# Kernel tuning notes

Hardware: AMD Instinct MI355X
Metric: run time of the kernel (lower is better)

The kernel has to match this reference:

```python
import jax, jax.numpy as jnp
import numpy as np

H, E, K, T_ENC = 512, 256, 256, 256  # hidden, embed, output_size(tags), max_length

def setup_inputs() -> dict:
    key = jax.random.key(0)
    ks = jax.random.split(key, 16)
    B, T = 128, 256
    s = 0.02
    return {
        "decoder_input": jax.random.randint(ks[0], (1, B, 1), 0, K),
        "output_tensor": jax.random.randint(ks[1], (T, B), 0, K),
        "encoder_outputs": jax.random.normal(ks[2], (T_ENC, B, 2 * H), dtype=jnp.float32),
        "emb": jax.random.normal(ks[3], (K, E), dtype=jnp.float32) * s,
        "attn_W": jax.random.normal(ks[4], (T_ENC, H + E), dtype=jnp.float32) * s,
        "attn_b": jnp.zeros((T_ENC,), jnp.float32),
        "comb_W": jax.random.normal(ks[5], (H, 2 * H + E), dtype=jnp.float32) * s,
        "comb_b": jnp.zeros((H,), jnp.float32),
        "gru_Wih": jax.random.normal(ks[6], (3 * H, H), dtype=jnp.float32) * s,
        "gru_Whh": jax.random.normal(ks[7], (3 * H, H), dtype=jnp.float32) * s,
        "gru_bih": jnp.zeros((3 * H,), jnp.float32),
        "gru_bhh": jnp.zeros((3 * H,), jnp.float32),
        "out_W": jax.random.normal(ks[8], (K, H), dtype=jnp.float32) * s,
        "out_b": jnp.zeros((K,), jnp.float32),
        "crf_start": jax.random.normal(ks[9], (K,), dtype=jnp.float32) * 0.1,
        "crf_end": jax.random.normal(ks[10], (K,), dtype=jnp.float32) * 0.1,
        "crf_trans": jax.random.normal(ks[11], (K, K), dtype=jnp.float32) * 0.1,
    }

def reference(decoder_input, output_tensor, encoder_outputs, emb, attn_W, attn_b,
              comb_W, comb_b, gru_Wih, gru_Whh, gru_bih, gru_bhh, out_W, out_b,
              crf_start, crf_end, crf_trans):
    B = decoder_input.shape[1]
    enc = jnp.transpose(encoder_outputs, (1, 0, 2))  # (B, T_enc, 2H)

    def dec_step(carry, true_t):
        dec_in, h = carry  # (B,), (B,H)
        e = emb[dec_in]  # (B,E)  (dropout_p=0 -> identity)
        aw = jax.nn.softmax(jnp.concatenate([e, h], axis=1) @ attn_W.T + attn_b, axis=1)  # (B,T_enc)
        ctx = jnp.einsum('bt,bth->bh', aw, enc)  # (B,2H)
        x = jax.nn.relu(jnp.concatenate([e, ctx], axis=1) @ comb_W.T + comb_b)  # (B,H)
        gi = x @ gru_Wih.T + gru_bih
        gh = h @ gru_Whh.T + gru_bhh
        ir, iz, inn = jnp.split(gi, 3, axis=1)
        hr, hz, hn = jnp.split(gh, 3, axis=1)
        r = jax.nn.sigmoid(ir + hr)
        z = jax.nn.sigmoid(iz + hz)
        n = jnp.tanh(inn + r * hn)
        h_new = (1.0 - z) * n + z * h
        logits = h_new @ out_W.T + out_b  # (B,K)
        return (true_t, h_new), logits  # teacher forcing: next input = true tag

    init = (decoder_input.reshape(B), jnp.zeros((B, H), encoder_outputs.dtype))
    _, emissions = jax.lax.scan(dec_step, init, output_tensor)  # (T,B,K)

    tags = output_tensor  # (T,B)
    em_score = jnp.take_along_axis(emissions, tags[:, :, None], axis=2)[..., 0].sum(0)  # (B,)
    numerator = crf_start[tags[0]] + em_score + crf_trans[tags[:-1], tags[1:]].sum(0) + crf_end[tags[-1]]

    def crf_fwd(score, em_t):  # score (B,K)
        score = jax.nn.logsumexp(score[:, :, None] + crf_trans[None] + em_t[:, None, :], axis=1)
        return score, None
    score0 = crf_start[None, :] + emissions[0]
    score, _ = jax.lax.scan(crf_fwd, score0, emissions[1:])
    denominator = jax.nn.logsumexp(score + crf_end[None, :], axis=1)  # (B,)

    llh = numerator - denominator
    return jnp.mean(llh)  # torchcrf reduction='mean'
```

## Files before the change

### kernel.cpp

```cpp
#include <hip/hip_runtime.h>


typedef unsigned short u16;
typedef unsigned int u32;
typedef __attribute__((ext_vector_type(8))) short short8;
typedef __attribute__((ext_vector_type(4))) float f32x4;
typedef __attribute__((ext_vector_type(4))) u32 u32x4;
typedef __attribute__((ext_vector_type(2))) u32 u32x2;

#define MFMA16(a, b, c) __builtin_amdgcn_mfma_f32_16x16x32_bf16((a), (b), (c), 0, 0, 0)

#define U_ENC 0u
#define U_WHH 16777216u
#define U_WIH 17563648u
#define U_WAW 18350080u
#define U_WOW 18546688u
#define U_WCE 18677760u
#define U_WXT 18808832u
#define U_HB  18874368u
#define U_EB  18939904u
#define U_XB  18972672u
#define U_PB  19038208u
#define F_LGB 9535488u
#define F_EMB 9568256u
#define F_EPB 9601024u
#define F_GHB 9666560u
#define F_SRB 9863168u
#define F_MFB 9895936u
#define F_NEB 9896064u
#define F_NSB 9896192u
#define F_BAR 9896448u
#define BAR_N 198147u

__device__ __forceinline__ float bf2f(u16 u) { return __uint_as_float(((u32)u) << 16); }
__device__ __forceinline__ u16 f2bf(float f) {
  u32 u = __float_as_uint(f);
  return (u16)((u + 0x7FFFu + ((u >> 16) & 1u)) >> 16);
}
__device__ __forceinline__ u32 pk2(float a, float b) {
  return (u32)f2bf(a) | ((u32)f2bf(b) << 16);
}

__device__ __forceinline__ float ldcg_f(const float* p) {
  float r;
  asm volatile("global_load_dword %0, %1, off sc0 sc1\n\ts_waitcnt vmcnt(0)"
               : "=v"(r) : "v"(p));
  return r;
}
__device__ __forceinline__ f32x4 ldcg_f4(const float* p) {
  f32x4 r;
  asm volatile("global_load_dwordx4 %0, %1, off sc0 sc1\n\ts_waitcnt vmcnt(0)"
               : "=v"(r) : "v"(p));
  return r;
}
__device__ __forceinline__ u32x2 ldcg_b8(const u16* p) {
  u32x2 r;
  asm volatile("global_load_dwordx2 %0, %1, off sc0 sc1\n\ts_waitcnt vmcnt(0)"
               : "=v"(r) : "v"(p));
  return r;
}
__device__ __forceinline__ void ldcg_f4x3(f32x4& a, f32x4& b, f32x4& c,
                                          const float* p0, const float* p1,
                                          const float* p2) {
  asm volatile(
      "global_load_dwordx4 %0, %3, off sc0 sc1\n\t"
      "global_load_dwordx4 %1, %4, off sc0 sc1\n\t"
      "global_load_dwordx4 %2, %5, off sc0 sc1\n\t"
      "s_waitcnt vmcnt(0)"
      : "=&v"(a), "=&v"(b), "=&v"(c)
      : "v"(p0), "v"(p1), "v"(p2));
}
__device__ __forceinline__ void ldcg8(u32x4 d[8], const u16* p) {
  asm volatile(
      "global_load_dwordx4 %0, %8, off sc0 sc1\n\t"
      "global_load_dwordx4 %1, %8, off offset:64 sc0 sc1\n\t"
      "global_load_dwordx4 %2, %8, off offset:128 sc0 sc1\n\t"
      "global_load_dwordx4 %3, %8, off offset:192 sc0 sc1\n\t"
      "global_load_dwordx4 %4, %8, off offset:256 sc0 sc1\n\t"
      "global_load_dwordx4 %5, %8, off offset:320 sc0 sc1\n\t"
      "global_load_dwordx4 %6, %8, off offset:384 sc0 sc1\n\t"
      "global_load_dwordx4 %7, %8, off offset:448 sc0 sc1\n\t"
      "s_waitcnt vmcnt(0)"
      : "=&v"(d[0]), "=&v"(d[1]), "=&v"(d[2]), "=&v"(d[3]),
        "=&v"(d[4]), "=&v"(d[5]), "=&v"(d[6]), "=&v"(d[7])
      : "v"(p));
}
__device__ __forceinline__ void ldcg16(u32x4 d[16], const u16* p) {
  asm volatile(
      "global_load_dwordx4 %0, %16, off sc0 sc1\n\t"
      "global_load_dwordx4 %1, %16, off offset:64 sc0 sc1\n\t"
      "global_load_dwordx4 %2, %16, off offset:128 sc0 sc1\n\t"
      "global_load_dwordx4 %3, %16, off offset:192 sc0 sc1\n\t"
      "global_load_dwordx4 %4, %16, off offset:256 sc0 sc1\n\t"
      "global_load_dwordx4 %5, %16, off offset:320 sc0 sc1\n\t"
      "global_load_dwordx4 %6, %16, off offset:384 sc0 sc1\n\t"
      "global_load_dwordx4 %7, %16, off offset:448 sc0 sc1\n\t"
      "global_load_dwordx4 %8, %16, off offset:512 sc0 sc1\n\t"
      "global_load_dwordx4 %9, %16, off offset:576 sc0 sc1\n\t"
      "global_load_dwordx4 %10, %16, off offset:640 sc0 sc1\n\t"
      "global_load_dwordx4 %11, %16, off offset:704 sc0 sc1\n\t"
      "global_load_dwordx4 %12, %16, off offset:768 sc0 sc1\n\t"
      "global_load_dwordx4 %13, %16, off offset:832 sc0 sc1\n\t"
      "global_load_dwordx4 %14, %16, off offset:896 sc0 sc1\n\t"
      "global_load_dwordx4 %15, %16, off offset:960 sc0 sc1\n\t"
      "s_waitcnt vmcnt(0)"
      : "=&v"(d[0]), "=&v"(d[1]), "=&v"(d[2]), "=&v"(d[3]),
        "=&v"(d[4]), "=&v"(d[5]), "=&v"(d[6]), "=&v"(d[7]),
        "=&v"(d[8]), "=&v"(d[9]), "=&v"(d[10]), "=&v"(d[11]),
        "=&v"(d[12]), "=&v"(d[13]), "=&v"(d[14]), "=&v"(d[15])
      : "v"(p));
}
__device__ __forceinline__ void stcg_f(float* p, float v) {
  asm volatile("global_store_dword %0, %1, off sc0 sc1" ::"v"(p), "v"(v) : "memory");
}
__device__ __forceinline__ void stcg_f4(float* p, f32x4 v) {
  asm volatile("global_store_dwordx4 %0, %1, off sc0 sc1" ::"v"(p), "v"(v) : "memory");
}
__device__ __forceinline__ void stcg_b8(u16* p, u32x2 v) {
  asm volatile("global_store_dwordx2 %0, %1, off sc0 sc1" ::"v"(p), "v"(v) : "memory");
}

__device__ __forceinline__ void gbar2(u32* bar, u32 gen, int grp) {
  __syncthreads();
  if (threadIdx.x == 0) {
    u32* l1 = bar + ((size_t)gen * 16u + (u32)grp) * 16u;
    u32* rel = bar + 197376u + gen;
    const u32 old = __hip_atomic_fetch_add(l1, 1u, __ATOMIC_RELAXED,
                                           __HIP_MEMORY_SCOPE_AGENT);
    if (old == 15u)
      __hip_atomic_fetch_add(rel, 1u, __ATOMIC_RELAXED, __HIP_MEMORY_SCOPE_AGENT);
    while (__hip_atomic_load(rel, __ATOMIC_RELAXED, __HIP_MEMORY_SCOPE_AGENT) < 16u) {}
  }
  __syncthreads();
}

__global__ void __launch_bounds__(256) kPrep(const float* __restrict__ wih,
                                             const float* __restrict__ whh,
                                             const float* __restrict__ aW,
                                             const float* __restrict__ oW,
                                             const float* __restrict__ cW,
                                             const float* __restrict__ ct,
                                             float* __restrict__ ws) {
  u16* W = (u16*)ws;
  const u32 i = blockIdx.x * 256 + threadIdx.x;
  if (i < 786432u) {
    W[U_WHH + i] = f2bf(whh[i]);
  } else if (i < 1572864u) {
    const u32 j = i - 786432u;
    W[U_WIH + j] = f2bf(wih[j]);
  } else if (i < 1769472u) {
    const u32 j = i - 1572864u;
    W[U_WAW + j] = f2bf(aW[j]);
  } else if (i < 1900544u) {
    const u32 j = i - 1769472u;
    W[U_WOW + j] = f2bf(oW[j]);
  } else if (i < 2031616u) {
    const u32 j = i - 1900544u;
    W[U_WCE + j] = f2bf(cW[(size_t)(j >> 8) * 1280 + (j & 255u)]);
  } else {
    const u32 j = i - 2031616u;
    const u32 kn = j >> 8, k = j & 255u;
    W[U_WXT + j] = f2bf(__expf(ct[k * 256u + kn]));
  }
}

__global__ void __launch_bounds__(256) kInit(const int* __restrict__ dec,
                                             const int* __restrict__ tags,
                                             const float* __restrict__ emb,
                                             const float* __restrict__ cs,
                                             const float* __restrict__ ce,
                                             const float* __restrict__ ct,
                                             float* __restrict__ ws) {
  const u32 idx = blockIdx.x * 256 + threadIdx.x;
  u16* ENC = (u16*)ws;
  u16* HB = ENC + U_HB;
  u16* EB = ENC + U_EB;
  if (idx < 32768u) {
    ((u32*)HB)[idx] = 0u;
    const int b = idx >> 8, j = idx & 255;
    EB[idx] = f2bf(emb[(size_t)dec[b] * 256 + j]);
  }
  if (idx < 128u) {
    int prev = tags[idx];
    float a = cs[prev];
    for (int t = 1; t < 256; ++t) {
      const int cur = tags[t * 128 + idx];
      a += ct[prev * 256 + cur];
      prev = cur;
    }
    ws[F_NSB + idx] = a + ce[prev];
    ws[F_NEB + idx] = 0.f;
  }
  u32* bar = (u32*)(ws + F_BAR);
  if (idx < 49537u) {
#pragma unroll
    for (int j = 0; j < 4; ++j) {
      const u32 k = idx * 4u + (u32)j;
      if (k < BAR_N) bar[k] = 0u;
    }
  }
}

__global__ void __launch_bounds__(256) kEncW(const float* __restrict__ enc,
                                             const float* __restrict__ cW,
                                             u16* __restrict__ encT) {
  __shared__ float wL[64 * 64];
  const int t = blockIdx.x >> 3, cblk = blockIdx.x & 7;
  const int tid = threadIdx.x;
  const int bg = tid & 31;
  const int cg = tid >> 5;
  float acc[4][8];
#pragma unroll
  for (int i = 0; i < 4; ++i)
#pragma unroll
    for (int c = 0; c < 8; ++c) acc[i][c] = 0.f;
  const float* encB = enc + (size_t)t * (128 * 1024);
  for (int jt = 0; jt < 16; ++jt) {
    const int j0 = jt * 64;
    __syncthreads();
    for (int i = tid; i < 4096; i += 256) {
      const int cc = i >> 6, jj = i & 63;
      wL[cc * 64 + jj] = cW[(size_t)(cblk * 64 + cc) * 1280 + 256 + j0 + jj];
    }
    __syncthreads();
    for (int jj = 0; jj < 64; ++jj) {
      const float e0 = encB[(bg * 4 + 0) * 1024 + j0 + jj];
      const float e1 = encB[(bg * 4 + 1) * 1024 + j0 + jj];
      const float e2 = encB[(bg * 4 + 2) * 1024 + j0 + jj];
      const float e3 = encB[(bg * 4 + 3) * 1024 + j0 + jj];
#pragma unroll
      for (int c = 0; c < 8; ++c) {
        const float wv = wL[(cg * 8 + c) * 64 + jj];
        acc[0][c] = fmaf(e0, wv, acc[0][c]);
        acc[1][c] = fmaf(e1, wv, acc[1][c]);
        acc[2][c] = fmaf(e2, wv, acc[2][c]);
        acc[3][c] = fmaf(e3, wv, acc[3][c]);
      }
    }
  }
#pragma unroll
  for (int i = 0; i < 4; ++i)
    for (int c = 0; c < 8; ++c) {
      const int b = bg * 4 + i, cc = cblk * 64 + cg * 8 + c;
      encT[(size_t)b * 131072u + (size_t)t * 512u + cc] = f2bf(acc[i][c]);
    }
}

struct P9 {
  const int* dec; const int* tags; const float* emb;
  const float* ab; const float* cb; const float* bih; const float* bhh;
  const float* ob; const float* cs;
  float* ws;
};

__global__ void __launch_bounds__(512, 2) maink(P9 p) {
  float* const ws = p.ws;
  u16* const ENC = (u16*)ws;
  const u16* const WHH16 = ENC + U_WHH;
  const u16* const WIH16 = ENC + U_WIH;
  const u16* const WAW16 = ENC + U_WAW;
  const u16* const WOW16 = ENC + U_WOW;
  const u16* const WCE16 = ENC + U_WCE;
  const u16* const WXT16 = ENC + U_WXT;
  u16* const HB = ENC + U_HB;
  u16* const EB = ENC + U_EB;
  u16* const XB = ENC + U_XB;
  u16* const PBu = ENC + U_PB;
  float* const LGB = ws + F_LGB;
  float* const EMB = ws + F_EMB;
  float* const EPB = ws + F_EPB;
  float* const GHB = ws + F_GHB;
  float* const SRB = ws + F_SRB;
  float* const MFB = ws + F_MFB;
  float* const NEB = ws + F_NEB;
  u32* const bar = (u32*)(ws + F_BAR);

  __shared__ float prL[256];
  __shared__ float pacc[4][256];
  __shared__ float red[16];
  __shared__ float pr3[3][256];

  const int tid = threadIdx.x;
  const int w = tid >> 6, lane = tid & 63;
  const int bq = lane & 15, kg = lane >> 4;
  const int blk = blockIdx.x;
  const int grp = blk >> 4;
  u32 gen = 0;

  for (int s = 0; s <= 256; ++s) {
    if (w < 3) {
      if (s < 256) {
        const int t = w * 256 + blk;
        const int r0 = (t >> 3) * 16, b0 = (t & 7) * 16;
        f32x4 acc;
        const float4 bs = *(const float4*)(p.bhh + r0 + kg * 4);
        acc[0] = bs.x; acc[1] = bs.y; acc[2] = bs.z; acc[3] = bs.w;
        u32x4 Bf[16];
        ldcg16(Bf, HB + (size_t)(b0 + bq) * 512 + kg * 8);
        const u16* Ar = WHH16 + (size_t)(r0 + bq) * 512 + kg * 8;
#pragma unroll
        for (int kt = 0; kt < 16; ++kt)
          acc = MFMA16(*(const short8*)(Ar + kt * 32),
                       __builtin_bit_cast(short8, Bf[kt]), acc);
        stcg_f4(GHB + (size_t)(b0 + bq) * 1536 + r0 + kg * 4, acc);
      }
    } else if (w == 3) {
      if (blk < 128) {
        if (s < 256) {
          const int r0 = (blk >> 3) * 16, b0 = (blk & 7) * 16;
          f32x4 acc;
          const float4 bs = *(const float4*)(p.ab + r0 + kg * 4);
          acc[0] = bs.x; acc[1] = bs.y; acc[2] = bs.z; acc[3] = bs.w;
          u32x4 Ef[8], Hf[16];
          ldcg8(Ef, EB + (size_t)(b0 + bq) * 256 + kg * 8);
          ldcg16(Hf, HB + (size_t)(b0 + bq) * 512 + kg * 8);
          const u16* Ar = WAW16 + (size_t)(r0 + bq) * 768 + kg * 8;
#pragma unroll
          for (int kt = 0; kt < 8; ++kt)
            acc = MFMA16(*(const short8*)(Ar + kt * 32),
                         __builtin_bit_cast(short8, Ef[kt]), acc);
#pragma unroll
          for (int kt = 0; kt < 16; ++kt)
            acc = MFMA16(*(const short8*)(Ar + 256 + kt * 32),
                         __builtin_bit_cast(short8, Hf[kt]), acc);
          stcg_f4(LGB + (size_t)(b0 + bq) * 256 + r0 + kg * 4, acc);
        }
      } else {
        if (s >= 1) {
          const int t2 = blk - 128;
          const int r0 = (t2 >> 3) * 16, b0 = (t2 & 7) * 16;
          f32x4 acc;
          const float4 bs = *(const float4*)(p.ob + r0 + kg * 4);
          acc[0] = bs.x; acc[1] = bs.y; acc[2] = bs.z; acc[3] = bs.w;
          u32x4 Hf[16];
          ldcg16(Hf, HB + (size_t)(b0 + bq) * 512 + kg * 8);
          const u16* Ar = WOW16 + (size_t)(r0 + bq) * 512 + kg * 8;
#pragma unroll
          for (int kt = 0; kt < 16; ++kt)
            acc = MFMA16(*(const short8*)(Ar + kt * 32),
                         __builtin_bit_cast(short8, Hf[kt]), acc);
          stcg_f4(EMB + (size_t)(b0 + bq) * 256 + r0 + kg * 4, acc);
        }
      }
    } else if (w == 4) {
      if (s < 256) {
        const int r0 = (blk >> 3) * 16, b0 = (blk & 7) * 16;
        f32x4 acc;
        const float4 bs = *(const float4*)(p.cb + r0 + kg * 4);
        acc[0] = bs.x; acc[1] = bs.y; acc[2] = bs.z; acc[3] = bs.w;
        u32x4 Ef[8];
        ldcg8(Ef, EB + (size_t)(b0 + bq) * 256 + kg * 8);
        const u16* Ar = WCE16 + (size_t)(r0 + bq) * 256 + kg * 8;
#pragma unroll
        for (int kt = 0; kt < 8; ++kt)
          acc = MFMA16(*(const short8*)(Ar + kt * 32),
                       __builtin_bit_cast(short8, Ef[kt]), acc);
        stcg_f4(EPB + (size_t)(b0 + bq) * 512 + r0 + kg * 4, acc);
      }
    } else if (w == 5) {
      if (blk < 128 && s >= 2) {
        const int b = blk;
        const f32x4 sv = ldcg_f4(SRB + (size_t)b * 256 + lane * 4);
        float mx = fmaxf(fmaxf(sv[0], sv[1]), fmaxf(sv[2], sv[3]));
#pragma unroll
        for (int o = 32; o; o >>= 1) mx = fmaxf(mx, __shfl_xor(mx, o));
        u32x2 pv;
        pv[0] = pk2(__expf(sv[0] - mx), __expf(sv[1] - mx));
        pv[1] = pk2(__expf(sv[2] - mx), __expf(sv[3] - mx));
        stcg_b8(PBu + (size_t)b * 256 + lane * 4, pv);
        if (lane == 0) stcg_f(MFB + b, mx);
      }
    }
    gbar2(bar, gen++, grp);

    {
      const int b = blk & 127, chalf = blk >> 7;
      if (s < 256) {
        float v = -3.0e38f;
        if (tid < 256) v = ldcg_f(LGB + (size_t)b * 256 + tid);
        float m = v;
#pragma unroll
        for (int o = 32; o; o >>= 1) m = fmaxf(m, __shfl_xor(m, o));
        if (lane == 0) red[w] = m;
        __syncthreads();
        float mB = red[0];
#pragma unroll
        for (int q = 1; q < 8; ++q) mB = fmaxf(mB, red[q]);
        float e = 0.f;
        if (tid < 256) { e = __expf(v - mB); prL[tid] = e; }
        float sacc = e;
#pragma unroll
        for (int o = 32; o; o >>= 1) sacc += __shfl_xor(sacc, o);
        if (lane == 0) red[8 + w] = sacc;
        __syncthreads();
        float sum = red[8];
#pragma unroll
        for (int q = 1; q < 8; ++q) sum += red[8 + q];
        const float inv = 1.f / sum;
        const int tq = tid >> 7, cp = tid & 127;
        const int c0l = cp * 2;
        const u16* base = ENC + (size_t)b * 131072u + (size_t)(tq * 64) * 512u +
                          (chalf * 256 + c0l);
        const float* prh = prL + tq * 64;
        float a0 = 0.f, a1 = 0.f;
#pragma unroll 8
        for (int t = 0; t < 64; ++t) {
          const float prt = prh[t];
          const u32 vv = __builtin_nontemporal_load((const u32*)(base + (size_t)t * 512));
          a0 = fmaf(prt, bf2f((u16)(vv & 0xffffu)), a0);
          a1 = fmaf(prt, bf2f((u16)(vv >> 16)), a1);
        }
        pacc[tq][c0l] = a0;
        pacc[tq][c0l + 1] = a1;
        __syncthreads();
        if (tid < 64) {
          const int cl = tid * 4;
          const f32x4 ep4 = ldcg_f4(EPB + (size_t)b * 512 + chalf * 256 + cl);
          float xv[4];
#pragma unroll
          for (int r = 0; r < 4; ++r)
            xv[r] = fmaxf(ep4[r] + (pacc[0][cl + r] + pacc[1][cl + r] +
                                    pacc[2][cl + r] + pacc[3][cl + r]) * inv, 0.f);
          u32x2 xo;
          xo[0] = pk2(xv[0], xv[1]);
          xo[1] = pk2(xv[2], xv[3]);
          stcg_b8(XB + (size_t)b * 512 + chalf * 256 + cl, xo);
        }
      }
      if (chalf == 0 && s >= 1 && tid == 0) {
        const int tg = p.tags[(s - 1) * 128 + b];
        const float em = ldcg_f(EMB + (size_t)b * 256 + tg);
        const float ne = ldcg_f(NEB + b);
        stcg_f(NEB + b, ne + em);
      }
    }
    gbar2(bar, gen++, grp);

    f32x4 R, Z, N;
    const bool giact = (s < 256) && (w == 0 || w == 2);
    if (giact) {
      const int r0 = (blk >> 3) * 16, b0 = (blk & 7) * 16;
      const int kh = w >> 1;
      if (kh == 0) {
        const float4 b1 = *(const float4*)(p.bih + r0 + kg * 4);
        const float4 b2 = *(const float4*)(p.bih + 512 + r0 + kg * 4);
        const float4 b3 = *(const float4*)(p.bih + 1024 + r0 + kg * 4);
        R[0] = b1.x; R[1] = b1.y; R[2] = b1.z; R[3] = b1.w;
        Z[0] = b2.x; Z[1] = b2.y; Z[2] = b2.z; Z[3] = b2.w;
        N[0] = b3.x; N[1] = b3.y; N[2] = b3.z; N[3] = b3.w;
      } else {
        R = (f32x4){0.f, 0.f, 0.f, 0.f}; Z = R; N = R;
      }
      u32x4 Xf[8];
      ldcg8(Xf, XB + (size_t)(b0 + bq) * 512 + kh * 256 + kg * 8);
      const u16* ArR = WIH16 + (size_t)(r0 + bq) * 512 + kh * 256 + kg * 8;
      const u16* ArZ = ArR + (size_t)512 * 512;
      const u16* ArN = ArR + (size_t)1024 * 512;
#pragma unroll
      for (int kt = 0; kt < 8; ++kt) {
        const short8 bb = __builtin_bit_cast(short8, Xf[kt]);
        R = MFMA16(*(const short8*)(ArR + kt * 32), bb, R);
        Z = MFMA16(*(const short8*)(ArZ + kt * 32), bb, Z);
        N = MFMA16(*(const short8*)(ArN + kt * 32), bb, N);
      }
      if (w == 2) {
#pragma unroll
        for (int r = 0; r < 4; ++r) {
          pr3[0][(kg * 4 + r) * 16 + bq] = R[r];
          pr3[1][(kg * 4 + r) * 16 + bq] = Z[r];
          pr3[2][(kg * 4 + r) * 16 + bq] = N[r];
        }
      }
    }
    __syncthreads();
    if (s < 256 && w == 0) {
      const int r0 = (blk >> 3) * 16, b0 = (blk & 7) * 16;
      const int b = b0 + bq;
      f32x4 gr4, gz4, gn4;
      ldcg_f4x3(gr4, gz4, gn4,
                GHB + (size_t)b * 1536 + r0 + kg * 4,
                GHB + (size_t)b * 1536 + 512 + r0 + kg * 4,
                GHB + (size_t)b * 1536 + 1024 + r0 + kg * 4);
      const u32x2 h4 = ldcg_b8(HB + (size_t)b * 512 + r0 + kg * 4);
      const float hold[4] = {bf2f((u16)(h4[0] & 0xffffu)), bf2f((u16)(h4[0] >> 16)),
                             bf2f((u16)(h4[1] & 0xffffu)), bf2f((u16)(h4[1] >> 16))};
      float hn[4];
#pragma unroll
      for (int r = 0; r < 4; ++r) {
        const float Rv = R[r] + pr3[0][(kg * 4 + r) * 16 + bq];
        const float Zv = Z[r] + pr3[1][(kg * 4 + r) * 16 + bq];
        const float Nv = N[r] + pr3[2][(kg * 4 + r) * 16 + bq];
        const float rr = 1.f / (1.f + __expf(-(Rv + gr4[r])));
        const float zz = 1.f / (1.f + __expf(-(Zv + gz4[r])));
        const float nn = tanhf(Nv + rr * gn4[r]);
        hn[r] = (1.f - zz) * nn + zz * hold[r];
      }
      u32x2 ho;
      ho[0] = pk2(hn[0], hn[1]);
      ho[1] = pk2(hn[2], hn[3]);
      stcg_b8(HB + (size_t)b * 512 + r0 + kg * 4, ho);
    }
    if (w == 1) {
      if (blk < 128) {
        if (s >= 1) {
          const int kn0 = (blk >> 3) * 16, b0 = (blk & 7) * 16;
          const int b = b0 + bq;
          if (s == 1) {
            const f32x4 e4 = ldcg_f4(EMB + (size_t)b * 256 + kn0 + kg * 4);
            const float4 c4 = *(const float4*)(p.cs + kn0 + kg * 4);
            f32x4 o;
            o[0] = c4.x + e4[0]; o[1] = c4.y + e4[1];
            o[2] = c4.z + e4[2]; o[3] = c4.w + e4[3];
            stcg_f4(SRB + (size_t)b * 256 + kn0 + kg * 4, o);
          } else {
            f32x4 acc = (f32x4){0.f, 0.f, 0.f, 0.f};
            u32x4 Pf[8];
            ldcg8(Pf, PBu + (size_t)(b0 + bq) * 256 + kg * 8);
            const u16* Ar = WXT16 + (size_t)(kn0 + bq) * 256 + kg * 8;
#pragma unroll
            for (int kt = 0; kt < 8; ++kt)
              acc = MFMA16(*(const short8*)(Ar + kt * 32),
                           __builtin_bit_cast(short8, Pf[kt]), acc);
            const float mf = ldcg_f(MFB + b);
            const f32x4 e4 = ldcg_f4(EMB + (size_t)b * 256 + kn0 + kg * 4);
            f32x4 o;
            o[0] = mf + __logf(acc[0]) + e4[0];
            o[1] = mf + __logf(acc[1]) + e4[1];
            o[2] = mf + __logf(acc[2]) + e4[2];
            o[3] = mf + __logf(acc[3]) + e4[3];
            stcg_f4(SRB + (size_t)b * 256 + kn0 + kg * 4, o);
          }
        }
      } else {
        if (s < 255) {
          const int b = blk - 128;
          const int tok = p.tags[s * 128 + b];
          const float4 ev = *(const float4*)(p.emb + (size_t)tok * 256 + lane * 4);
          u32x2 ee;
          ee[0] = pk2(ev.x, ev.y);
          ee[1] = pk2(ev.z, ev.w);
          stcg_b8(EB + (size_t)b * 256 + lane * 4, ee);
        }
      }
    }
    gbar2(bar, gen++, grp);
  }
}

__global__ void __launch_bounds__(128) kFinal(const float* __restrict__ ws,
                                              const float* __restrict__ ce,
                                              float* __restrict__ out) {
  __shared__ float acc[128];
  const int tid = threadIdx.x;
  const float* SRB = ws + F_SRB;
  float mx = -3.0e38f;
#pragma unroll 8
  for (int k = 0; k < 256; ++k) mx = fmaxf(mx, SRB[(size_t)tid * 256 + k] + ce[k]);
  float sm = 0.f;
#pragma unroll 8
  for (int k = 0; k < 256; ++k) sm += __expf(SRB[(size_t)tid * 256 + k] + ce[k] - mx);
  acc[tid] = ws[F_NSB + tid] + ws[F_NEB + tid] - (mx + __logf(sm));
  __syncthreads();
  if (tid < 64) {
    float v = acc[tid] + acc[tid + 64];
#pragma unroll
    for (int o = 32; o; o >>= 1) v += __shfl_xor(v, o);
    if (tid == 0) out[0] = v * (1.f / 128.f);
  }
}

extern "C" void kernel_launch(void* const* d_in, const int* in_sizes, int n_in,
                              void* d_out, int out_size, void* d_ws, size_t ws_size,
                              hipStream_t stream) {
  (void)in_sizes; (void)n_in; (void)out_size; (void)ws_size;
  const int* dec = (const int*)d_in[0];
  const int* tags = (const int*)d_in[1];
  const float* enc = (const float*)d_in[2];
  const float* emb = (const float*)d_in[3];
  const float* aW = (const float*)d_in[4];
  const float* ab = (const float*)d_in[5];
  const float* cW = (const float*)d_in[6];
  const float* cb = (const float*)d_in[7];
  const float* wih = (const float*)d_in[8];
  const float* whh = (const float*)d_in[9];
  const float* bih = (const float*)d_in[10];
  const float* bhh = (const float*)d_in[11];
  const float* oW = (const float*)d_in[12];
  const float* ob = (const float*)d_in[13];
  const float* cs = (const float*)d_in[14];
  const float* ce = (const float*)d_in[15];
  const float* ct = (const float*)d_in[16];
  float* ws = (float*)d_ws;
  float* out = (float*)d_out;

  kPrep<<<dim3(8192), dim3(256), 0, stream>>>(wih, whh, aW, oW, cW, ct, ws);
  kInit<<<dim3(256), dim3(256), 0, stream>>>(dec, tags, emb, cs, ce, ct, ws);
  kEncW<<<dim3(2048), dim3(256), 0, stream>>>(enc, cW, (u16*)d_ws);

  P9 p;
  p.dec = dec; p.tags = tags; p.emb = emb;
  p.ab = ab; p.cb = cb; p.bih = bih; p.bhh = bhh;
  p.ob = ob; p.cs = cs; p.ws = ws;
  void* args[] = { &p };
  hipLaunchCooperativeKernel((void*)maink, dim3(256), dim3(512), args, 0, stream);

  kFinal<<<dim3(1), dim3(128), 0, stream>>>(ws, ce, out);
}
```

Measured before the change: 8.678 ms.

## Rebalance persistent decoder phases across blocks and add group-flag barrier release

Redistributes per-step work in the persistent kernel. The Whh matvec moves into the attention phase on blocks 128+, and comb-embedding and CRF-normalize work shift into the first phase. The attention context is now computed by a single block per batch row using all 8 waves with wide register-prefetched encoder loads, instead of two half-blocks. The global barrier now has only the group leader spin on the release counter, then publish a per-group flag that the other blocks poll, cutting contention on one address. The emission accumulation moves to the last phase. These changes add register pressure and change phase ordering, which carries a risk of data-race bugs.

Result: slower. 9.894 ms (+14.0%).

```diff
diff --git a/kernel.cpp b/kernel.cpp
--- a/kernel.cpp
+++ b/kernel.cpp
@@ -30,7 +30,9 @@
 #define F_NEB 9896064u
 #define F_NSB 9896192u
 #define F_BAR 9896448u
-#define BAR_N 198147u
+#define REL_OFF 197376u
+#define GF_OFF 198147u
+#define BAR_N 198403u
 
 __device__ __forceinline__ float bf2f(u16 u) { return __uint_as_float(((u32)u) << 16); }
 __device__ __forceinline__ u16 f2bf(float f) {
@@ -119,17 +121,27 @@
 __device__ __forceinline__ void stcg_b8(u16* p, u32x2 v) {
   asm volatile("global_store_dwordx2 %0, %1, off sc0 sc1" ::"v"(p), "v"(v) : "memory");
 }
-
-__device__ __forceinline__ void gbar2(u32* bar, u32 gen, int grp) {
+__device__ __forceinline__ void stcg_h(u16* p, u32 v) {
+  asm volatile("global_store_short %0, %1, off sc0 sc1" ::"v"(p), "v"(v) : "memory");
+}
+
+__device__ __forceinline__ void gbar2(u32* bar, u32 gen, int blk) {
   __syncthreads();
   if (threadIdx.x == 0) {
-    u32* l1 = bar + ((size_t)gen * 16u + (u32)grp) * 16u;
-    u32* rel = bar + 197376u + gen;
+    const u32 grp = (u32)(blk >> 4);
+    u32* l1 = bar + ((size_t)gen * 16u + grp) * 16u;
+    u32* rel = bar + REL_OFF + gen;
+    u32* gf = bar + GF_OFF + grp * 16u;
     const u32 old = __hip_atomic_fetch_add(l1, 1u, __ATOMIC_RELAXED,
                                            __HIP_MEMORY_SCOPE_AGENT);
     if (old == 15u)
       __hip_atomic_fetch_add(rel, 1u, __ATOMIC_RELAXED, __HIP_MEMORY_SCOPE_AGENT);
-    while (__hip_atomic_load(rel, __ATOMIC_RELAXED, __HIP_MEMORY_SCOPE_AGENT) < 16u) {}
+    if ((blk & 15) == 0) {
+      while (__hip_atomic_load(rel, __ATOMIC_RELAXED, __HIP_MEMORY_SCOPE_AGENT) < 16u) {}
+      __hip_atomic_store(gf, gen + 1u, __ATOMIC_RELAXED, __HIP_MEMORY_SCOPE_AGENT);
+    } else {
+      while (__hip_atomic_load(gf, __ATOMIC_RELAXED, __HIP_MEMORY_SCOPE_AGENT) < gen + 1u) {}
+    }
   }
   __syncthreads();
 }
@@ -192,7 +204,7 @@
     ws[F_NEB + idx] = 0.f;
   }
   u32* bar = (u32*)(ws + F_BAR);
-  if (idx < 49537u) {
+  if (idx < 49601u) {
 #pragma unroll
     for (int j = 0; j < 4; ++j) {
       const u32 k = idx * 4u + (u32)j;
@@ -275,37 +287,18 @@
   float* const NEB = ws + F_NEB;
   u32* const bar = (u32*)(ws + F_BAR);
 
-  __shared__ float prL[256];
-  __shared__ float pacc[4][256];
-  __shared__ float red[16];
+  __shared__ float PL[8 * 576];
   __shared__ float pr3[3][256];
 
   const int tid = threadIdx.x;
   const int w = tid >> 6, lane = tid & 63;
   const int bq = lane & 15, kg = lane >> 4;
   const int blk = blockIdx.x;
-  const int grp = blk >> 4;
   u32 gen = 0;
 
   for (int s = 0; s <= 256; ++s) {
-    if (w < 3) {
-      if (s < 256) {
-        const int t = w * 256 + blk;
-        const int r0 = (t >> 3) * 16, b0 = (t & 7) * 16;
-        f32x4 acc;
-        const float4 bs = *(const float4*)(p.bhh + r0 + kg * 4);
-        acc[0] = bs.x; acc[1] = bs.y; acc[2] = bs.z; acc[3] = bs.w;
-        u32x4 Bf[16];
-        ldcg16(Bf, HB + (size_t)(b0 + bq) * 512 + kg * 8);
-        const u16* Ar = WHH16 + (size_t)(r0 + bq) * 512 + kg * 8;
-#pragma unroll
-        for (int kt = 0; kt < 16; ++kt)
-          acc = MFMA16(*(const short8*)(Ar + kt * 32),
-                       __builtin_bit_cast(short8, Bf[kt]), acc);
-        stcg_f4(GHB + (size_t)(b0 + bq) * 1536 + r0 + kg * 4, acc);
-      }
-    } else if (w == 3) {
-      if (blk < 128) {
+    if (blk < 128) {
+      if (w == 0) {
         if (s < 256) {
           const int r0 = (blk >> 3) * 16, b0 = (blk & 7) * 16;
           f32x4 acc;
@@ -325,9 +318,105 @@
                          __builtin_bit_cast(short8, Hf[kt]), acc);
           stcg_f4(LGB + (size_t)(b0 + bq) * 256 + r0 + kg * 4, acc);
         }
-      } else {
+      } else if (w == 5) {
+        if (s >= 2) {
+          const int b = blk;
+          const f32x4 sv = ldcg_f4(SRB + (size_t)b * 256 + lane * 4);
+          float mx = fmaxf(fmaxf(sv[0], sv[1]), fmaxf(sv[2], sv[3]));
+#pragma unroll
+          for (int o = 32; o; o >>= 1) mx = fmaxf(mx, __shfl_xor(mx, o));
+          u32x2 pv;
+          pv[0] = pk2(__expf(sv[0] - mx), __expf(sv[1] - mx));
+          pv[1] = pk2(__expf(sv[2] - mx), __expf(sv[3] - mx));
+          stcg_b8(PBu + (size_t)b * 256 + lane * 4, pv);
+          if (lane == 0) stcg_f(MFB + b, mx);
+        }
+      }
+    } else {
+      if (w < 2 && s < 256) {
+        const int id = (blk - 128) * 2 + w;
+        const int r0 = (id >> 3) * 16, b0 = (id & 7) * 16;
+        f32x4 acc;
+        const float4 bs = *(const float4*)(p.cb + r0 + kg * 4);
+        acc[0] = bs.x; acc[1] = bs.y; acc[2] = bs.z; acc[3] = bs.w;
+        u32x4 Ef[8];
+        ldcg8(Ef, EB + (size_t)(b0 + bq) * 256 + kg * 8);
+        const u16* Ar = WCE16 + (size_t)(r0 + bq) * 256 + kg * 8;
+#pragma unroll
+        for (int kt = 0; kt < 8; ++kt)
+          acc = MFMA16(*(const short8*)(Ar + kt * 32),
+                       __builtin_bit_cast(short8, Ef[kt]), acc);
+        stcg_f4(EPB + (size_t)(b0 + bq) * 512 + r0 + kg * 4, acc);
+      }
+    }
+    gbar2(bar, gen++, blk);
+
+    if (blk < 128) {
+      if (s < 256) {
+        const int b = blk;
+        const f32x4 lg = ldcg_f4(LGB + (size_t)b * 256 + lane * 4);
+        const u16* sbase = ENC + (size_t)b * 131072u + (size_t)(w * 32) * 512u + lane * 8;
+        u32x4 dv[32];
+#pragma unroll
+        for (int j = 0; j < 32; ++j)
+          dv[j] = __builtin_nontemporal_load(
+              reinterpret_cast<const u32x4*>(sbase + (size_t)j * 512));
+        float m = fmaxf(fmaxf(lg[0], lg[1]), fmaxf(lg[2], lg[3]));
+#pragma unroll
+        for (int o = 32; o; o >>= 1) m = fmaxf(m, __shfl_xor(m, o));
+        f32x4 pr;
+        float sm = 0.f;
+#pragma unroll
+        for (int i = 0; i < 4; ++i) { pr[i] = __expf(lg[i] - m); sm += pr[i]; }
+#pragma unroll
+        for (int o = 32; o; o >>= 1) sm += __shfl_xor(sm, o);
+        const float inv = 1.f / sm;
+        float prr[32];
+#pragma unroll
+        for (int j = 0; j < 32; ++j)
+          prr[j] = __shfl(pr[j & 3], w * 8 + (j >> 2), 64);
+        float acc[8];
+#pragma unroll
+        for (int i = 0; i < 8; ++i) acc[i] = 0.f;
+#pragma unroll
+        for (int j = 0; j < 32; ++j) {
+          const u32x4 v = dv[j];
+#pragma unroll
+          for (int q = 0; q < 4; ++q) {
+            acc[2 * q] = fmaf(prr[j], bf2f((u16)(v[q] & 0xffffu)), acc[2 * q]);
+            acc[2 * q + 1] = fmaf(prr[j], bf2f((u16)(v[q] >> 16)), acc[2 * q + 1]);
+          }
+        }
+#pragma unroll
+        for (int i = 0; i < 8; ++i) PL[w * 576 + lane * 9 + i] = acc[i];
+        __syncthreads();
+        const int c = tid;
+        float s8 = 0.f;
+#pragma unroll
+        for (int ww = 0; ww < 8; ++ww) s8 += PL[ww * 576 + c + (c >> 3)];
+        const float xv = fmaxf(ldcg_f(EPB + (size_t)b * 512 + c) + s8 * inv, 0.f);
+        stcg_h(XB + (size_t)b * 512 + c, (u32)f2bf(xv));
+      }
+    } else {
+      const int id = (blk - 128) * 8 + w;
+      if (id < 768) {
+        if (s < 256) {
+          const int r0 = (id >> 3) * 16, b0 = (id & 7) * 16;
+          f32x4 acc;
+          const float4 bs = *(const float4*)(p.bhh + r0 + kg * 4);
+          acc[0] = bs.x; acc[1] = bs.y; acc[2] = bs.z; acc[3] = bs.w;
+          u32x4 Bf[16];
+          ldcg16(Bf, HB + (size_t)(b0 + bq) * 512 + kg * 8);
+          const u16* Ar = WHH16 + (size_t)(r0 + bq) * 512 + kg * 8;
+#pragma unroll
+          for (int kt = 0; kt < 16; ++kt)
+            acc = MFMA16(*(const short8*)(Ar + kt * 32),
+                         __builtin_bit_cast(short8, Bf[kt]), acc);
+          stcg_f4(GHB + (size_t)(b0 + bq) * 1536 + r0 + kg * 4, acc);
+        }
+      } else if (id < 896) {
         if (s >= 1) {
-          const int t2 = blk - 128;
+          const int t2 = id - 768;
           const int r0 = (t2 >> 3) * 16, b0 = (t2 & 7) * 16;
           f32x4 acc;
           const float4 bs = *(const float4*)(p.ob + r0 + kg * 4);
@@ -342,99 +431,8 @@
           stcg_f4(EMB + (size_t)(b0 + bq) * 256 + r0 + kg * 4, acc);
         }
       }
-    } else if (w == 4) {
-      if (s < 256) {
-        const int r0 = (blk >> 3) * 16, b0 = (blk & 7) * 16;
-        f32x4 acc;
-        const float4 bs = *(const float4*)(p.cb + r0 + kg * 4);
-        acc[0] = bs.x; acc[1] = bs.y; acc[2] = bs.z; acc[3] = bs.w;
-        u32x4 Ef[8];
-        ldcg8(Ef, EB + (size_t)(b0 + bq) * 256 + kg * 8);
-        const u16* Ar = WCE16 + (size_t)(r0 + bq) * 256 + kg * 8;
-#pragma unroll
-        for (int kt = 0; kt < 8; ++kt)
-          acc = MFMA16(*(const short8*)(Ar + kt * 32),
-                       __builtin_bit_cast(short8, Ef[kt]), acc);
-        stcg_f4(EPB + (size_t)(b0 + bq) * 512 + r0 + kg * 4, acc);
-      }
-    } else if (w == 5) {
-      if (blk < 128 && s >= 2) {
-        const int b = blk;
-        const f32x4 sv = ldcg_f4(SRB + (size_t)b * 256 + lane * 4);
-        float mx = fmaxf(fmaxf(sv[0], sv[1]), fmaxf(sv[2], sv[3]));
-#pragma unroll
-        for (int o = 32; o; o >>= 1) mx = fmaxf(mx, __shfl_xor(mx, o));
-        u32x2 pv;
-        pv[0] = pk2(__expf(sv[0] - mx), __expf(sv[1] - mx));
-        pv[1] = pk2(__expf(sv[2] - mx), __expf(sv[3] - mx));
-        stcg_b8(PBu + (size_t)b * 256 + lane * 4, pv);
-        if (lane == 0) stcg_f(MFB + b, mx);
-      }
-    }
-    gbar2(bar, gen++, grp);
-
-    {
-      const int b = blk & 127, chalf = blk >> 7;
-      if (s < 256) {
-        float v = -3.0e38f;
-        if (tid < 256) v = ldcg_f(LGB + (size_t)b * 256 + tid);
-        float m = v;
-#pragma unroll
-        for (int o = 32; o; o >>= 1) m = fmaxf(m, __shfl_xor(m, o));
-        if (lane == 0) red[w] = m;
-        __syncthreads();
-        float mB = red[0];
-#pragma unroll
-        for (int q = 1; q < 8; ++q) mB = fmaxf(mB, red[q]);
-        float e = 0.f;
-        if (tid < 256) { e = __expf(v - mB); prL[tid] = e; }
-        float sacc = e;
-#pragma unroll
-        for (int o = 32; o; o >>= 1) sacc += __shfl_xor(sacc, o);
-        if (lane == 0) red[8 + w] = sacc;
-        __syncthreads();
-        float sum = red[8];
-#pragma unroll
-        for (int q = 1; q < 8; ++q) sum += red[8 + q];
-        const float inv = 1.f / sum;
-        const int tq = tid >> 7, cp = tid & 127;
-        const int c0l = cp * 2;
-        const u16* base = ENC + (size_t)b * 131072u + (size_t)(tq * 64) * 512u +
-                          (chalf * 256 + c0l);
-        const float* prh = prL + tq * 64;
-        float a0 = 0.f, a1 = 0.f;
-#pragma unroll 8
-        for (int t = 0; t < 64; ++t) {
-          const float prt = prh[t];
-          const u32 vv = __builtin_nontemporal_load((const u32*)(base + (size_t)t * 512));
-          a0 = fmaf(prt, bf2f((u16)(vv & 0xffffu)), a0);
-          a1 = fmaf(prt, bf2f((u16)(vv >> 16)), a1);
-        }
-        pacc[tq][c0l] = a0;
-        pacc[tq][c0l + 1] = a1;
-        __syncthreads();
-        if (tid < 64) {
-          const int cl = tid * 4;
-          const f32x4 ep4 = ldcg_f4(EPB + (size_t)b * 512 + chalf * 256 + cl);
-          float xv[4];
-#pragma unroll
-          for (int r = 0; r < 4; ++r)
-            xv[r] = fmaxf(ep4[r] + (pacc[0][cl + r] + pacc[1][cl + r] +
-                                    pacc[2][cl + r] + pacc[3][cl + r]) * inv, 0.f);
-          u32x2 xo;
-          xo[0] = pk2(xv[0], xv[1]);
-          xo[1] = pk2(xv[2], xv[3]);
-          stcg_b8(XB + (size_t)b * 512 + chalf * 256 + cl, xo);
-        }
-      }
-      if (chalf == 0 && s >= 1 && tid == 0) {
-        const int tg = p.tags[(s - 1) * 128 + b];
-        const float em = ldcg_f(EMB + (size_t)b * 256 + tg);
-        const float ne = ldcg_f(NEB + b);
-        stcg_f(NEB + b, ne + em);
-      }
-    }
-    gbar2(bar, gen++, grp);
+    }
+    gbar2(bar, gen++, blk);
 
     f32x4 R, Z, N;
     const bool giact = (s < 256) && (w == 0 || w == 2);
@@ -543,7 +541,13 @@
         }
       }
     }
-    gbar2(bar, gen++, grp);
+    if (w == 3 && blk < 128 && s >= 1 && lane == 0) {
+      const int tg = p.tags[(s - 1) * 128 + blk];
+      const float em = ldcg_f(EMB + (size_t)blk * 256 + tg);
+      const float ne = ldcg_f(NEB + blk);
+      stcg_f(NEB + blk, ne + em);
+    }
+    gbar2(bar, gen++, blk);
   }
 }
 
```

## Prefetch encoder slice into registers during GEMM phase and restructure softmax-context

Applied to the files above, without the earlier changes.

Each wave now issues non-temporal loads of its 32-row slice of the bf16 encoder block for the current batch row before the first grid barrier, overlapping them with the MFMA phase. Partial s_waitcnt plus sched barriers let the GEMM inputs arrive without waiting for the prefetch. The attention softmax is reorganised so every wave redundantly computes max and sum with warp shuffles, dropping two block syncs. The context reduction is spread over 8 waves with 4 columns per lane, using registers and a padded LDS reduction. The cost is 64 extra VGPRs held across the barrier, which may reduce occupancy or cause spills.

Result: slower. 12.06 ms (+38.9%).

```diff
diff --git a/kernel.cpp b/kernel.cpp
--- a/kernel.cpp
+++ b/kernel.cpp
@@ -110,6 +110,61 @@
         "=&v"(d[12]), "=&v"(d[13]), "=&v"(d[14]), "=&v"(d[15])
       : "v"(p));
 }
+__device__ __forceinline__ f32x4 ldcg_f4_nw(const float* p) {
+  f32x4 r;
+  asm volatile("global_load_dwordx4 %0, %1, off sc0 sc1" : "=v"(r) : "v"(p));
+  return r;
+}
+__device__ __forceinline__ void ldcg8_nw(u32x4 d[8], const u16* p) {
+  asm volatile(
+      "global_load_dwordx4 %0, %8, off sc0 sc1\n\t"
+      "global_load_dwordx4 %1, %8, off offset:64 sc0 sc1\n\t"
+      "global_load_dwordx4 %2, %8, off offset:128 sc0 sc1\n\t"
+      "global_load_dwordx4 %3, %8, off offset:192 sc0 sc1\n\t"
+      "global_load_dwordx4 %4, %8, off offset:256 sc0 sc1\n\t"
+      "global_load_dwordx4 %5, %8, off offset:320 sc0 sc1\n\t"
+      "global_load_dwordx4 %6, %8, off offset:384 sc0 sc1\n\t"
+      "global_load_dwordx4 %7, %8, off offset:448 sc0 sc1"
+      : "=&v"(d[0]), "=&v"(d[1]), "=&v"(d[2]), "=&v"(d[3]),
+        "=&v"(d[4]), "=&v"(d[5]), "=&v"(d[6]), "=&v"(d[7])
+      : "v"(p));
+}
+__device__ __forceinline__ void ldcg16_nw(u32x4 d[16], const u16* p) {
+  asm volatile(
+      "global_load_dwordx4 %0, %16, off sc0 sc1\n\t"
+      "global_load_dwordx4 %1, %16, off offset:64 sc0 sc1\n\t"
+      "global_load_dwordx4 %2, %16, off offset:128 sc0 sc1\n\t"
+      "global_load_dwordx4 %3, %16, off offset:192 sc0 sc1\n\t"
+      "global_load_dwordx4 %4, %16, off offset:256 sc0 sc1\n\t"
+      "global_load_dwordx4 %5, %16, off offset:320 sc0 sc1\n\t"
+      "global_load_dwordx4 %6, %16, off offset:384 sc0 sc1\n\t"
+      "global_load_dwordx4 %7, %16, off offset:448 sc0 sc1\n\t"
+      "global_load_dwordx4 %8, %16, off offset:512 sc0 sc1\n\t"
+      "global_load_dwordx4 %9, %16, off offset:576 sc0 sc1\n\t"
+      "global_load_dwordx4 %10, %16, off offset:640 sc0 sc1\n\t"
+      "global_load_dwordx4 %11, %16, off offset:704 sc0 sc1\n\t"
+      "global_load_dwordx4 %12, %16, off offset:768 sc0 sc1\n\t"
+      "global_load_dwordx4 %13, %16, off offset:832 sc0 sc1\n\t"
+      "global_load_dwordx4 %14, %16, off offset:896 sc0 sc1\n\t"
+      "global_load_dwordx4 %15, %16, off offset:960 sc0 sc1"
+      : "=&v"(d[0]), "=&v"(d[1]), "=&v"(d[2]), "=&v"(d[3]),
+        "=&v"(d[4]), "=&v"(d[5]), "=&v"(d[6]), "=&v"(d[7]),
+        "=&v"(d[8]), "=&v"(d[9]), "=&v"(d[10]), "=&v"(d[11]),
+        "=&v"(d[12]), "=&v"(d[13]), "=&v"(d[14]), "=&v"(d[15])
+      : "v"(p));
+}
+__device__ __forceinline__ void ldnt4(u32x2 d[4], const u16* p) {
+  asm volatile(
+      "global_load_dwordx2 %0, %4, off nt\n\t"
+      "global_load_dwordx2 %1, %4, off offset:1024 nt\n\t"
+      "global_load_dwordx2 %2, %4, off offset:2048 nt\n\t"
+      "global_load_dwordx2 %3, %4, off offset:3072 nt"
+      : "=&v"(d[0]), "=&v"(d[1]), "=&v"(d[2]), "=&v"(d[3])
+      : "v"(p));
+}
+#define VMW32 do { asm volatile("s_waitcnt vmcnt(32)"); __builtin_amdgcn_sched_barrier(0); } while (0)
+#define VMW0  do { asm volatile("s_waitcnt vmcnt(0)");  __builtin_amdgcn_sched_barrier(0); } while (0)
+
 __device__ __forceinline__ void stcg_f(float* p, float v) {
   asm volatile("global_store_dword %0, %1, off sc0 sc1" ::"v"(p), "v"(v) : "memory");
 }
@@ -118,6 +173,14 @@
 }
 __device__ __forceinline__ void stcg_b8(u16* p, u32x2 v) {
   asm volatile("global_store_dwordx2 %0, %1, off sc0 sc1" ::"v"(p), "v"(v) : "memory");
+}
+
+__device__ __forceinline__ void prefetch_enc(u32x2 pf[32], const u16* ENC,
+                                             int blk, int w, int lane) {
+  const u16* pfb = ENC + (size_t)(blk & 127) * 131072u + (size_t)(w * 32) * 512u +
+                   ((blk >> 7) * 256) + lane * 4;
+#pragma unroll
+  for (int j8 = 0; j8 < 8; ++j8) ldnt4(pf + j8 * 4, pfb + j8 * 2048);
 }
 
 __device__ __forceinline__ void gbar2(u32* bar, u32 gen, int grp) {
@@ -275,9 +338,7 @@
   float* const NEB = ws + F_NEB;
   u32* const bar = (u32*)(ws + F_BAR);
 
-  __shared__ float prL[256];
-  __shared__ float pacc[4][256];
-  __shared__ float red[16];
+  __shared__ float PL[8 * 260];
   __shared__ float pr3[3][256];
 
   const int tid = threadIdx.x;
@@ -288,6 +349,8 @@
   u32 gen = 0;
 
   for (int s = 0; s <= 256; ++s) {
+    u32x2 pf[32];
+
     if (w < 3) {
       if (s < 256) {
         const int t = w * 256 + blk;
@@ -296,7 +359,9 @@
         const float4 bs = *(const float4*)(p.bhh + r0 + kg * 4);
         acc[0] = bs.x; acc[1] = bs.y; acc[2] = bs.z; acc[3] = bs.w;
         u32x4 Bf[16];
-        ldcg16(Bf, HB + (size_t)(b0 + bq) * 512 + kg * 8);
+        ldcg16_nw(Bf, HB + (size_t)(b0 + bq) * 512 + kg * 8);
+        prefetch_enc(pf, ENC, blk, w, lane);
+        VMW32;
         const u16* Ar = WHH16 + (size_t)(r0 + bq) * 512 + kg * 8;
 #pragma unroll
         for (int kt = 0; kt < 16; ++kt)
@@ -312,7 +377,7 @@
           const float4 bs = *(const float4*)(p.ab + r0 + kg * 4);
           acc[0] = bs.x; acc[1] = bs.y; acc[2] = bs.z; acc[3] = bs.w;
           u32x4 Ef[8], Hf[16];
-          ldcg8(Ef, EB + (size_t)(b0 + bq) * 256 + kg * 8);
+          ldcg8_nw(Ef, EB + (size_t)(b0 + bq) * 256 + kg * 8);
           ldcg16(Hf, HB + (size_t)(b0 + bq) * 512 + kg * 8);
           const u16* Ar = WAW16 + (size_t)(r0 + bq) * 768 + kg * 8;
 #pragma unroll
@@ -324,6 +389,7 @@
             acc = MFMA16(*(const short8*)(Ar + 256 + kt * 32),
                          __builtin_bit_cast(short8, Hf[kt]), acc);
           stcg_f4(LGB + (size_t)(b0 + bq) * 256 + r0 + kg * 4, acc);
+          prefetch_enc(pf, ENC, blk, w, lane);
         }
       } else {
         if (s >= 1) {
@@ -333,13 +399,16 @@
           const float4 bs = *(const float4*)(p.ob + r0 + kg * 4);
           acc[0] = bs.x; acc[1] = bs.y; acc[2] = bs.z; acc[3] = bs.w;
           u32x4 Hf[16];
-          ldcg16(Hf, HB + (size_t)(b0 + bq) * 512 + kg * 8);
+          ldcg16_nw(Hf, HB + (size_t)(b0 + bq) * 512 + kg * 8);
+          if (s < 256) { prefetch_enc(pf, ENC, blk, w, lane); VMW32; } else { VMW0; }
           const u16* Ar = WOW16 + (size_t)(r0 + bq) * 512 + kg * 8;
 #pragma unroll
           for (int kt = 0; kt < 16; ++kt)
             acc = MFMA16(*(const short8*)(Ar + kt * 32),
                          __builtin_bit_cast(short8, Hf[kt]), acc);
           stcg_f4(EMB + (size_t)(b0 + bq) * 256 + r0 + kg * 4, acc);
+        } else {
+          prefetch_enc(pf, ENC, blk, w, lane);
         }
       }
     } else if (w == 4) {
@@ -349,7 +418,9 @@
         const float4 bs = *(const float4*)(p.cb + r0 + kg * 4);
         acc[0] = bs.x; acc[1] = bs.y; acc[2] = bs.z; acc[3] = bs.w;
         u32x4 Ef[8];
-        ldcg8(Ef, EB + (size_t)(b0 + bq) * 256 + kg * 8);
+        ldcg8_nw(Ef, EB + (size_t)(b0 + bq) * 256 + kg * 8);
+        prefetch_enc(pf, ENC, blk, w, lane);
+        VMW32;
         const u16* Ar = WCE16 + (size_t)(r0 + bq) * 256 + kg * 8;
 #pragma unroll
         for (int kt = 0; kt < 8; ++kt)
@@ -360,7 +431,8 @@
     } else if (w == 5) {
       if (blk < 128 && s >= 2) {
         const int b = blk;
-        const f32x4 sv = ldcg_f4(SRB + (size_t)b * 256 + lane * 4);
+        const f32x4 sv = ldcg_f4_nw(SRB + (size_t)b * 256 + lane * 4);
+        if (s < 256) { prefetch_enc(pf, ENC, blk, w, lane); VMW32; } else { VMW0; }
         float mx = fmaxf(fmaxf(sv[0], sv[1]), fmaxf(sv[2], sv[3]));
 #pragma unroll
         for (int o = 32; o; o >>= 1) mx = fmaxf(mx, __shfl_xor(mx, o));
@@ -369,58 +441,60 @@
         pv[1] = pk2(__expf(sv[2] - mx), __expf(sv[3] - mx));
         stcg_b8(PBu + (size_t)b * 256 + lane * 4, pv);
         if (lane == 0) stcg_f(MFB + b, mx);
-      }
+      } else if (s < 256) {
+        prefetch_enc(pf, ENC, blk, w, lane);
+      }
+    } else {
+      if (s < 256) prefetch_enc(pf, ENC, blk, w, lane);
     }
     gbar2(bar, gen++, grp);
 
     {
       const int b = blk & 127, chalf = blk >> 7;
       if (s < 256) {
-        float v = -3.0e38f;
-        if (tid < 256) v = ldcg_f(LGB + (size_t)b * 256 + tid);
-        float m = v;
+        const f32x4 lg = ldcg_f4(LGB + (size_t)b * 256 + lane * 4);
+        float m = fmaxf(fmaxf(lg[0], lg[1]), fmaxf(lg[2], lg[3]));
 #pragma unroll
         for (int o = 32; o; o >>= 1) m = fmaxf(m, __shfl_xor(m, o));
-        if (lane == 0) red[w] = m;
-        __syncthreads();
-        float mB = red[0];
-#pragma unroll
-        for (int q = 1; q < 8; ++q) mB = fmaxf(mB, red[q]);
-        float e = 0.f;
-        if (tid < 256) { e = __expf(v - mB); prL[tid] = e; }
-        float sacc = e;
-#pragma unroll
-        for (int o = 32; o; o >>= 1) sacc += __shfl_xor(sacc, o);
-        if (lane == 0) red[8 + w] = sacc;
-        __syncthreads();
-        float sum = red[8];
-#pragma unroll
-        for (int q = 1; q < 8; ++q) sum += red[8 + q];
-        const float inv = 1.f / sum;
-        const int tq = tid >> 7, cp = tid & 127;
-        const int c0l = cp * 2;
-        const u16* base = ENC + (size_t)b * 131072u + (size_t)(tq * 64) * 512u +
-                          (chalf * 256 + c0l);
-        const float* prh = prL + tq * 64;
-        float a0 = 0.f, a1 = 0.f;
-#pragma unroll 8
-        for (int t = 0; t < 64; ++t) {
-          const float prt = prh[t];
-          const u32 vv = __builtin_nontemporal_load((const u32*)(base + (size_t)t * 512));
-          a0 = fmaf(prt, bf2f((u16)(vv & 0xffffu)), a0);
-          a1 = fmaf(prt, bf2f((u16)(vv >> 16)), a1);
+        f32x4 pr;
+        float sm = 0.f;
+#pragma unroll
+        for (int i = 0; i < 4; ++i) { pr[i] = __expf(lg[i] - m); sm += pr[i]; }
+#pragma unroll
+        for (int o = 32; o; o >>= 1) sm += __shfl_xor(sm, o);
+        const float inv = 1.f / sm;
+        float prr[32];
+#pragma unroll
+        for (int j = 0; j < 32; ++j)
+          prr[j] = __shfl(pr[j & 3], w * 8 + (j >> 2), 64);
+        VMW0;
+        float a0 = 0.f, a1 = 0.f, a2 = 0.f, a3 = 0.f;
+#pragma unroll
+        for (int j = 0; j < 32; ++j) {
+          const u32x2 v = pf[j];
+          a0 = fmaf(prr[j], bf2f((u16)(v[0] & 0xffffu)), a0);
+          a1 = fmaf(prr[j], bf2f((u16)(v[0] >> 16)), a1);
+          a2 = fmaf(prr[j], bf2f((u16)(v[1] & 0xffffu)), a2);
+          a3 = fmaf(prr[j], bf2f((u16)(v[1] >> 16)), a3);
         }
-        pacc[tq][c0l] = a0;
-        pacc[tq][c0l + 1] = a1;
+        float* PLw = PL + w * 260 + lane * 4;
+        PLw[0] = a0; PLw[1] = a1; PLw[2] = a2; PLw[3] = a3;
         __syncthreads();
         if (tid < 64) {
           const int cl = tid * 4;
+          f32x4 s8 = (f32x4){0.f, 0.f, 0.f, 0.f};
+#pragma unroll
+          for (int ww = 0; ww < 8; ++ww) {
+            s8[0] += PL[ww * 260 + cl];
+            s8[1] += PL[ww * 260 + cl + 1];
+            s8[2] += PL[ww * 260 + cl + 2];
+            s8[3] += PL[ww * 260 + cl + 3];
+          }
           const f32x4 ep4 = ldcg_f4(EPB + (size_t)b * 512 + chalf * 256 + cl);
           float xv[4];
 #pragma unroll
           for (int r = 0; r < 4; ++r)
-            xv[r] = fmaxf(ep4[r] + (pacc[0][cl + r] + pacc[1][cl + r] +
-                                    pacc[2][cl + r] + pacc[3][cl + r]) * inv, 0.f);
+            xv[r] = fmaxf(ep4[r] + s8[r] * inv, 0.f);
           u32x2 xo;
           xo[0] = pk2(xv[0], xv[1]);
           xo[1] = pk2(xv[2], xv[3]);
```
